# Optimization experiments

Hardware: AMD Instinct MI355X
Metric: run time of the kernel (lower is better)

The kernel has to match this reference:

```python
import jax, jax.numpy as jnp
import numpy as np

N = 8192
IN_F = 512
OUT_F = 64
ALPHA = 0.2  # LeakyReLU negative slope
NEG_INF = -9e15


def setup_inputs() -> dict:
    key = jax.random.key(0)
    k1, k2, k3, k4 = jax.random.split(key, 4)
    # xavier_uniform-style scale (gain=1.414)
    w_bound = 1.414 * np.sqrt(6.0 / (IN_F + OUT_F))
    a_bound = 1.414 * np.sqrt(6.0 / (2 * OUT_F + 1))
    return {
        "input": jax.random.normal(k1, (N, IN_F), dtype=jnp.float32),
        "adj": jax.random.randint(k2, (N, N), 0, 2, dtype=jnp.int32),
        "W": jax.random.uniform(k3, (IN_F, OUT_F), jnp.float32, -w_bound, w_bound),
        "a": jax.random.uniform(k4, (2 * OUT_F, 1), jnp.float32, -a_bound, a_bound),
        "sig_sample_size": 512,
    }


def reference(input, adj, W, a, sig_sample_size):
    h = input @ W  # [N, F]
    # Split 'a' so e_ij = leakyrelu(a1.h_i + a2.h_j) without the N*N*2F repeat/cat
    a1, a2 = a[:OUT_F, 0], a[OUT_F:, 0]  # [F], [F]
    e = jax.nn.leaky_relu((h @ a1)[:, None] + (h @ a2)[None, :], negative_slope=ALPHA)  # [N, N]
    attention = jnp.where(adj > 0, e, NEG_INF)
    attention = jax.nn.softmax(attention, axis=1)
    sig_scores = jnp.sum(attention, axis=0)  # [N]
    _, indices = jax.lax.top_k(sig_scores, sig_sample_size)
    return indices
```

## Files before the change

kernel.cpp:

```cpp
#include <hip/hip_runtime.h>
#include <stdint.h>

#define NROW 8192
#define IN_F 512
#define OUT_F 64
#define ALPHA 0.2f

typedef int int4e __attribute__((ext_vector_type(4)));

__device__ float  g_f1[NROW];
__device__ float  g_f2[NROW];
__device__ float  g_E2f[NROW];
__device__ float  g_F2f[NROW];
__device__ double g_E2d[NROW];
__device__ double g_F2d[NROW];
__device__ double g_accp[NROW];
__device__ double g_accn[NROW];
__device__ double g_colsum[NROW];
__device__ unsigned long long g_maskP[(size_t)NROW * 128];
__device__ unsigned long long g_maskN[(size_t)NROW * 128];

__global__ void __launch_bounds__(512) fused_f(const float* __restrict__ in,
                                               const float* __restrict__ W,
                                               const float* __restrict__ a) {
    __shared__ __align__(16) float wa1s[IN_F];
    __shared__ __align__(16) float wa2s[IN_F];
    int tid = threadIdx.x;
    {
        int k = tid;
        double s1 = 0.0, s2 = 0.0;
        for (int t = 0; t < OUT_F; ++t) {
            double w = (double)W[k * OUT_F + t];
            s1 += w * (double)a[t];
            s2 += w * (double)a[OUT_F + t];
        }
        wa1s[k] = (float)s1;
        wa2s[k] = (float)s2;
    }
    if (tid < 8) g_colsum[blockIdx.x * 8 + tid] = 0.0;
    __syncthreads();
    int wave = tid >> 6, lane = tid & 63;
    int row = blockIdx.x * 8 + wave;
    const float4* in4  = (const float4*)(in + (size_t)row * IN_F);
    const float4* wa14 = (const float4*)wa1s;
    const float4* wa24 = (const float4*)wa2s;
    double s1 = 0.0, s2 = 0.0;
    #pragma unroll
    for (int half = 0; half < 2; ++half) {
        int idx = half * 64 + lane;
        float4 x = in4[idx];
        float4 u = wa14[idx];
        float4 v = wa24[idx];
        s1 += (double)x.x*u.x + (double)x.y*u.y + (double)x.z*u.z + (double)x.w*u.w;
        s2 += (double)x.x*v.x + (double)x.y*v.y + (double)x.z*v.z + (double)x.w*v.w;
    }
    #pragma unroll
    for (int off = 32; off > 0; off >>= 1) {
        s1 += __shfl_down(s1, off, 64);
        s2 += __shfl_down(s2, off, 64);
    }
    if (lane == 0) {
        float f1 = (float)s1, f2 = (float)s2;
        g_f1[row] = f1; g_f2[row] = f2;
        double e2 = exp((double)f2), g2 = exp(0.2 * (double)f2);
        g_E2d[row] = e2;        g_F2d[row] = g2;
        g_E2f[row] = (float)e2; g_F2f[row] = (float)g2;
    }
}

__global__ void __launch_bounds__(256, 2) row_z_mask(const int* __restrict__ adj) {
    __shared__ float E2s[NROW];
    __shared__ float F2s[NROW];
    __shared__ double zp[16], zn[16];
    int tid = threadIdx.x;
    int wave = tid >> 6, lane = tid & 63;
    for (int k = tid; k < NROW / 4; k += 256) {
        ((float4*)E2s)[k] = ((const float4*)g_E2f)[k];
        ((float4*)F2s)[k] = ((const float4*)g_F2f)[k];
    }
    __syncthreads();
    int row0 = blockIdx.x * 4;
    for (int r = 0; r < 4; ++r) {
        int row = row0 + r;
        float f1r = g_f1[row];
        float Ft = expf(-0.2f * f1r);
        const int4e* arow = (const int4e*)(adj + (size_t)row * NROW) + wave * 512;
        int4e av[8];
        #pragma unroll
        for (int it = 0; it < 8; ++it) av[it] = arow[it * 64 + lane];
        unsigned long long mywordP = 0, mywordN = 0;
        double accp = 0.0, accn = 0.0;
        #pragma unroll
        for (int it = 0; it < 8; ++it) {
            int colbase = wave * 2048 + it * 256 + lane * 4;
            float4 E2v = *(const float4*)&E2s[colbase];
            float4 F2v = *(const float4*)&F2s[colbase];
            bool p0 = av[it].x > 0, p1 = av[it].y > 0;
            bool p2 = av[it].z > 0, p3 = av[it].w > 0;
            bool q0 = F2v.x > Ft, q1 = F2v.y > Ft, q2 = F2v.z > Ft, q3 = F2v.w > Ft;
            unsigned long long bp0 = __ballot(p0 && q0),  bn0 = __ballot(p0 && !q0);
            unsigned long long bp1 = __ballot(p1 && q1),  bn1 = __ballot(p1 && !q1);
            unsigned long long bp2 = __ballot(p2 && q2),  bn2 = __ballot(p2 && !q2);
            unsigned long long bp3 = __ballot(p3 && q3),  bn3 = __ballot(p3 && !q3);
            int bl = it * 4;
            if (lane == bl)     { mywordP = bp0; mywordN = bn0; }
            if (lane == bl + 1) { mywordP = bp1; mywordN = bn1; }
            if (lane == bl + 2) { mywordP = bp2; mywordN = bn2; }
            if (lane == bl + 3) { mywordP = bp3; mywordN = bn3; }
            accp += (p0 && q0) ? (double)E2v.x : 0.0;
            accn += (p0 && !q0) ? (double)F2v.x : 0.0;
            accp += (p1 && q1) ? (double)E2v.y : 0.0;
            accn += (p1 && !q1) ? (double)F2v.y : 0.0;
            accp += (p2 && q2) ? (double)E2v.z : 0.0;
            accn += (p2 && !q2) ? (double)F2v.z : 0.0;
            accp += (p3 && q3) ? (double)E2v.w : 0.0;
            accn += (p3 && !q3) ? (double)F2v.w : 0.0;
        }
        if (lane < 32) {
            g_maskP[(size_t)row * 128 + wave * 32 + lane] = mywordP;
            g_maskN[(size_t)row * 128 + wave * 32 + lane] = mywordN;
        }
        #pragma unroll
        for (int off = 32; off > 0; off >>= 1) {
            accp += __shfl_down(accp, off, 64);
            accn += __shfl_down(accn, off, 64);
        }
        if (lane == 0) { zp[r * 4 + wave] = accp; zn[r * 4 + wave] = accn; }
    }
    __syncthreads();
    if (tid < 4) {
        g_accp[row0 + tid] = zp[tid*4+0] + zp[tid*4+1] + zp[tid*4+2] + zp[tid*4+3];
        g_accn[row0 + tid] = zn[tid*4+0] + zn[tid*4+1] + zn[tid*4+2] + zn[tid*4+3];
    }
}

__device__ __forceinline__ unsigned long long btr64(unsigned long long x, int lane) {
    const unsigned long long hm[6] = {
        0xAAAAAAAAAAAAAAAAULL, 0xCCCCCCCCCCCCCCCCULL, 0xF0F0F0F0F0F0F0F0ULL,
        0xFF00FF00FF00FF00ULL, 0xFFFF0000FFFF0000ULL, 0xFFFFFFFF00000000ULL };
    #pragma unroll
    for (int s = 0; s < 6; ++s) {
        int d = 1 << s;
        unsigned long long y = __shfl_xor(x, d, 64);
        unsigned long long hi = hm[s];
        x = (lane & d) ? ((x & hi) | ((y >> d) & ~hi))
                       : ((x & ~hi) | ((y << d) & hi));
    }
    return x;
}

__global__ void __launch_bounds__(256) colsum_kernel() {
    __shared__ double2 GHs[256];
    int tid = threadIdx.x;
    int w = tid >> 6, lane = tid & 63;
    int cb = blockIdx.x & 31;
    int rb = blockIdx.x >> 5;
    int i0 = rb * 256;
    {
        float f1v = g_f1[i0 + tid];
        double e1 = exp((double)f1v), h1 = exp(0.2 * (double)f1v);
        double Z = e1 * g_accp[i0 + tid] + h1 * g_accn[i0 + tid];
        double zi = 1.0 / Z;
        GHs[tid] = make_double2(e1 * zi, h1 * zi);
    }
    __syncthreads();
    int glo[4], ghi[4], hlo[4], hhi[4];
    #pragma unroll
    for (int t = 0; t < 4; ++t) {
        double2 gh = GHs[t * 64 + lane];
        glo[t] = __double2loint(gh.x); ghi[t] = __double2hiint(gh.x);
        hlo[t] = __double2loint(gh.y); hhi[t] = __double2hiint(gh.y);
    }
    int W = cb * 4 + w;
    unsigned long long TP[4], TN[4];
    #pragma unroll
    for (int t = 0; t < 4; ++t) {
        unsigned long long xp = g_maskP[(size_t)(i0 + t * 64 + lane) * 128 + W];
        unsigned long long xn = g_maskN[(size_t)(i0 + t * 64 + lane) * 128 + W];
        TP[t] = btr64(xp, lane);
        TN[t] = btr64(xn, lane);
    }
    int j = (W >> 5) * 2048 + ((W >> 2) & 7) * 256 + lane * 4 + (W & 3);
    double accp = 0.0, accn = 0.0;
    #pragma unroll
    for (int t = 0; t < 4; ++t) {
        unsigned long long wp = TP[t], wn = TN[t];
        int a0 = glo[t], a1 = ghi[t], b0 = hlo[t], b1 = hhi[t];
        for (int s = 0; s < 64; ++s) {
            double G1i = __hiloint2double(__builtin_amdgcn_readlane(a1, s),
                                          __builtin_amdgcn_readlane(a0, s));
            double H1i = __hiloint2double(__builtin_amdgcn_readlane(b1, s),
                                          __builtin_amdgcn_readlane(b0, s));
            accp += ((wp >> s) & 1ULL) ? G1i : 0.0;
            accn += ((wn >> s) & 1ULL) ? H1i : 0.0;
        }
    }
    double res = g_E2d[j] * accp + g_F2d[j] * accn;
    atomicAdd(&g_colsum[j], res);
}

__global__ void __launch_bounds__(1024) topk_kernel(int* __restrict__ out, int K) {
    __shared__ unsigned int sbits[NROW];
    __shared__ unsigned int hist[256];
    __shared__ unsigned long long cand[1024];
    __shared__ unsigned long long s_prefix;
    __shared__ unsigned int s_want, s_cnt;
    int tid = threadIdx.x;
    int lane = tid & 63;
    for (int k = tid; k < NROW; k += 1024) {
        float s = (float)g_colsum[k];
        unsigned int u = __float_as_uint(s);
        u = (u & 0x80000000u) ? ~u : (u | 0x80000000u);
        sbits[k] = u;
    }
    if (tid == 0) { s_prefix = 0ULL; s_want = (unsigned)K; s_cnt = 0; }
    __syncthreads();
    for (int lvl = 0; lvl < 6; ++lvl) {
        int shift = 40 - lvl * 8;
        if (tid < 256) hist[tid] = 0;
        __syncthreads();
        unsigned long long pmask = (lvl == 0) ? 0ULL : (~0ULL << (shift + 8));
        unsigned long long prefix = s_prefix;
        for (int k = tid; k < NROW; k += 1024) {
            unsigned long long kk =
                ((unsigned long long)sbits[k] << 13) | (unsigned long long)(8191 - k);
            bool match = ((kk & pmask) == prefix);
            unsigned bb = (unsigned)(kk >> shift) & 255u;
            unsigned long long act = __ballot(match);
            unsigned long long same = act;
            #pragma unroll
            for (int t = 0; t < 8; ++t) {
                unsigned long long bt = __ballot((bb >> t) & 1u);
                same &= ((bb >> t) & 1u) ? bt : ~bt;
            }
            if (match) {
                int lead = __ffsll((long long)same) - 1;
                if (lane == lead) atomicAdd(&hist[bb], (unsigned)__popcll(same));
            }
        }
        __syncthreads();
        if (tid == 0) {
            unsigned cum = 0; int b = 255;
            for (; b >= 0; --b) { cum += hist[b]; if (cum >= s_want) break; }
            if (b < 0) b = 0;
            s_want -= (cum - hist[b]);
            s_prefix |= ((unsigned long long)b << shift);
        }
        __syncthreads();
    }
    unsigned long long thr = s_prefix;
    for (int k = tid; k < NROW; k += 1024) {
        unsigned long long kk =
            ((unsigned long long)sbits[k] << 13) | (unsigned long long)(8191 - k);
        bool keep = (kk >= thr);
        unsigned long long m = __ballot(keep);
        if (m) {
            int lead = __ffsll((long long)m) - 1;
            unsigned base = 0;
            if (lane == lead) base = atomicAdd(&s_cnt, (unsigned)__popcll(m));
            base = (unsigned)__shfl((int)base, lead, 64);
            if (keep) {
                unsigned pos = base + (unsigned)__popcll(m & ((1ULL << lane) - 1ULL));
                if (pos < 1024u) cand[pos] = kk;
            }
        }
    }
    __syncthreads();
    unsigned cnt = s_cnt;
    if ((unsigned)tid >= cnt) cand[tid] = 0ULL;
    __syncthreads();
    for (int k2 = 2; k2 <= 1024; k2 <<= 1) {
        for (int jj = k2 >> 1; jj > 0; jj >>= 1) {
            int ixj = tid ^ jj;
            if (ixj > tid) {
                unsigned long long a = cand[tid], b = cand[ixj];
                bool up = ((tid & k2) == 0);
                if (up ? (a < b) : (a > b)) { cand[tid] = b; cand[ixj] = a; }
            }
            __syncthreads();
        }
    }
    if (tid < K) out[tid] = 8191 - (int)(cand[tid] & 0x1FFFULL);
}

extern "C" void kernel_launch(void* const* d_in, const int* in_sizes, int n_in,
                              void* d_out, int out_size, void* d_ws, size_t ws_size,
                              hipStream_t stream) {
    const float* input = (const float*)d_in[0];
    const int*   adj   = (const int*)d_in[1];
    const float* W     = (const float*)d_in[2];
    const float* a     = (const float*)d_in[3];
    int* out = (int*)d_out;
    int K = out_size;

    fused_f<<<NROW / 8, 512, 0, stream>>>(input, W, a);
    row_z_mask<<<NROW / 4, 256, 0, stream>>>(adj);
    colsum_kernel<<<1024, 256, 0, stream>>>();
    topk_kernel<<<1, 1024, 0, stream>>>(out, K);
}
```

Measured before the change: 563.3 us.

## Split adjacency mask streaming from row sums and store a single mask

The row pass now streams only the adjacency and writes one bitmask instead of separate positive and negative masks. Row normalizers are computed in a new kernel that reads the mask and a permuted E/F table from shared memory. The column-sum kernel recomputes the sign of f1+f2 per element instead of loading a second mask. This halves mask write and read traffic and lightens the adjacency-streaming kernel, at the cost of two extra launches and more per-element ALU work in colsum. The sign test also changes from a comparison of exponentials to a direct sum comparison, which could classify boundary cases differently.

```diff
diff --git a/kernel.cpp b/kernel.cpp
--- a/kernel.cpp
+++ b/kernel.cpp
@@ -17,8 +17,8 @@
 __device__ double g_accp[NROW];
 __device__ double g_accn[NROW];
 __device__ double g_colsum[NROW];
-__device__ unsigned long long g_maskP[(size_t)NROW * 128];
-__device__ unsigned long long g_maskN[(size_t)NROW * 128];
+__device__ unsigned long long g_mask[(size_t)NROW * 128];
+__device__ float2 g_EFp[NROW];
 
 __global__ void __launch_bounds__(512) fused_f(const float* __restrict__ in,
                                                const float* __restrict__ W,
@@ -68,70 +68,83 @@
     }
 }
 
-__global__ void __launch_bounds__(256, 2) row_z_mask(const int* __restrict__ adj) {
-    __shared__ float E2s[NROW];
-    __shared__ float F2s[NROW];
-    __shared__ double zp[16], zn[16];
+__global__ void tbl_perm() {
+    int idx = blockIdx.x * 256 + threadIdx.x;
+    int W = idx >> 6, l = idx & 63;
+    int j = (W >> 5) * 2048 + ((W >> 2) & 7) * 256 + l * 4 + (W & 3);
+    g_EFp[idx] = make_float2(g_E2f[j], g_F2f[j]);
+}
+
+__global__ void __launch_bounds__(256) mask_stream(const int* __restrict__ adj) {
     int tid = threadIdx.x;
     int wave = tid >> 6, lane = tid & 63;
-    for (int k = tid; k < NROW / 4; k += 256) {
-        ((float4*)E2s)[k] = ((const float4*)g_E2f)[k];
-        ((float4*)F2s)[k] = ((const float4*)g_F2f)[k];
-    }
-    __syncthreads();
     int row0 = blockIdx.x * 4;
     for (int r = 0; r < 4; ++r) {
         int row = row0 + r;
-        float f1r = g_f1[row];
-        float Ft = expf(-0.2f * f1r);
         const int4e* arow = (const int4e*)(adj + (size_t)row * NROW) + wave * 512;
         int4e av[8];
         #pragma unroll
         for (int it = 0; it < 8; ++it) av[it] = arow[it * 64 + lane];
-        unsigned long long mywordP = 0, mywordN = 0;
-        double accp = 0.0, accn = 0.0;
+        unsigned long long myword = 0;
         #pragma unroll
         for (int it = 0; it < 8; ++it) {
-            int colbase = wave * 2048 + it * 256 + lane * 4;
-            float4 E2v = *(const float4*)&E2s[colbase];
-            float4 F2v = *(const float4*)&F2s[colbase];
-            bool p0 = av[it].x > 0, p1 = av[it].y > 0;
-            bool p2 = av[it].z > 0, p3 = av[it].w > 0;
-            bool q0 = F2v.x > Ft, q1 = F2v.y > Ft, q2 = F2v.z > Ft, q3 = F2v.w > Ft;
-            unsigned long long bp0 = __ballot(p0 && q0),  bn0 = __ballot(p0 && !q0);
-            unsigned long long bp1 = __ballot(p1 && q1),  bn1 = __ballot(p1 && !q1);
-            unsigned long long bp2 = __ballot(p2 && q2),  bn2 = __ballot(p2 && !q2);
-            unsigned long long bp3 = __ballot(p3 && q3),  bn3 = __ballot(p3 && !q3);
+            unsigned long long b0 = __ballot(av[it].x > 0);
+            unsigned long long b1 = __ballot(av[it].y > 0);
+            unsigned long long b2 = __ballot(av[it].z > 0);
+            unsigned long long b3 = __ballot(av[it].w > 0);
             int bl = it * 4;
-            if (lane == bl)     { mywordP = bp0; mywordN = bn0; }
-            if (lane == bl + 1) { mywordP = bp1; mywordN = bn1; }
-            if (lane == bl + 2) { mywordP = bp2; mywordN = bn2; }
-            if (lane == bl + 3) { mywordP = bp3; mywordN = bn3; }
-            accp += (p0 && q0) ? (double)E2v.x : 0.0;
-            accn += (p0 && !q0) ? (double)F2v.x : 0.0;
-            accp += (p1 && q1) ? (double)E2v.y : 0.0;
-            accn += (p1 && !q1) ? (double)F2v.y : 0.0;
-            accp += (p2 && q2) ? (double)E2v.z : 0.0;
-            accn += (p2 && !q2) ? (double)F2v.z : 0.0;
-            accp += (p3 && q3) ? (double)E2v.w : 0.0;
-            accn += (p3 && !q3) ? (double)F2v.w : 0.0;
-        }
-        if (lane < 32) {
-            g_maskP[(size_t)row * 128 + wave * 32 + lane] = mywordP;
-            g_maskN[(size_t)row * 128 + wave * 32 + lane] = mywordN;
-        }
-        #pragma unroll
-        for (int off = 32; off > 0; off >>= 1) {
-            accp += __shfl_down(accp, off, 64);
-            accn += __shfl_down(accn, off, 64);
-        }
-        if (lane == 0) { zp[r * 4 + wave] = accp; zn[r * 4 + wave] = accn; }
-    }
-    __syncthreads();
-    if (tid < 4) {
-        g_accp[row0 + tid] = zp[tid*4+0] + zp[tid*4+1] + zp[tid*4+2] + zp[tid*4+3];
-        g_accn[row0 + tid] = zn[tid*4+0] + zn[tid*4+1] + zn[tid*4+2] + zn[tid*4+3];
-    }
+            if (lane == bl)     myword = b0;
+            if (lane == bl + 1) myword = b1;
+            if (lane == bl + 2) myword = b2;
+            if (lane == bl + 3) myword = b3;
+        }
+        if (lane < 32) g_mask[(size_t)row * 128 + wave * 32 + lane] = myword;
+    }
+}
+
+__global__ void __launch_bounds__(1024) rowsum_kernel() {
+    __shared__ float2 EF[NROW];
+    int tid = threadIdx.x;
+    int wave = tid >> 6, lane = tid & 63;
+    for (int k = tid; k < NROW; k += 1024) EF[k] = g_EFp[k];
+    __syncthreads();
+    int row = blockIdx.x * 16 + wave;
+    float f1r = g_f1[row];
+    float Ft = expf(-0.2f * f1r);
+    unsigned long long wlo = g_mask[(size_t)row * 128 + lane];
+    unsigned long long whi = g_mask[(size_t)row * 128 + 64 + lane];
+    int wl0 = (int)(unsigned)wlo,        wl1 = (int)(unsigned)(wlo >> 32);
+    int wh0 = (int)(unsigned)whi,        wh1 = (int)(unsigned)(whi >> 32);
+    double accp = 0.0, accn = 0.0;
+    int half = lane >> 5, bit = lane & 31;
+    #pragma unroll
+    for (int w = 0; w < 64; ++w) {
+        unsigned lo = (unsigned)__builtin_amdgcn_readlane(wl0, w);
+        unsigned hi = (unsigned)__builtin_amdgcn_readlane(wl1, w);
+        unsigned sel = half ? hi : lo;
+        bool b = (sel >> bit) & 1u;
+        float2 ef = EF[w * 64 + lane];
+        bool q = ef.y > Ft;
+        accp += (b && q)  ? (double)ef.x : 0.0;
+        accn += (b && !q) ? (double)ef.y : 0.0;
+    }
+    #pragma unroll
+    for (int w = 0; w < 64; ++w) {
+        unsigned lo = (unsigned)__builtin_amdgcn_readlane(wh0, w);
+        unsigned hi = (unsigned)__builtin_amdgcn_readlane(wh1, w);
+        unsigned sel = half ? hi : lo;
+        bool b = (sel >> bit) & 1u;
+        float2 ef = EF[(64 + w) * 64 + lane];
+        bool q = ef.y > Ft;
+        accp += (b && q)  ? (double)ef.x : 0.0;
+        accn += (b && !q) ? (double)ef.y : 0.0;
+    }
+    #pragma unroll
+    for (int off = 32; off > 0; off >>= 1) {
+        accp += __shfl_down(accp, off, 64);
+        accn += __shfl_down(accn, off, 64);
+    }
+    if (lane == 0) { g_accp[row] = accp; g_accn[row] = accn; }
 }
 
 __device__ __forceinline__ unsigned long long btr64(unsigned long long x, int lane) {
@@ -151,48 +164,54 @@
 
 __global__ void __launch_bounds__(256) colsum_kernel() {
     __shared__ double2 GHs[256];
+    __shared__ float   f1sh[256];
     int tid = threadIdx.x;
     int w = tid >> 6, lane = tid & 63;
     int cb = blockIdx.x & 31;
     int rb = blockIdx.x >> 5;
     int i0 = rb * 256;
+    float f1v = g_f1[i0 + tid];
+    f1sh[tid] = f1v;
     {
-        float f1v = g_f1[i0 + tid];
         double e1 = exp((double)f1v), h1 = exp(0.2 * (double)f1v);
         double Z = e1 * g_accp[i0 + tid] + h1 * g_accn[i0 + tid];
         double zi = 1.0 / Z;
         GHs[tid] = make_double2(e1 * zi, h1 * zi);
     }
     __syncthreads();
-    int glo[4], ghi[4], hlo[4], hhi[4];
+    int glo[4], ghi[4], hlo[4], hhi[4], fbits[4];
     #pragma unroll
     for (int t = 0; t < 4; ++t) {
         double2 gh = GHs[t * 64 + lane];
         glo[t] = __double2loint(gh.x); ghi[t] = __double2hiint(gh.x);
         hlo[t] = __double2loint(gh.y); hhi[t] = __double2hiint(gh.y);
+        fbits[t] = __float_as_int(f1sh[t * 64 + lane]);
     }
     int W = cb * 4 + w;
-    unsigned long long TP[4], TN[4];
+    unsigned long long TP[4];
     #pragma unroll
     for (int t = 0; t < 4; ++t) {
-        unsigned long long xp = g_maskP[(size_t)(i0 + t * 64 + lane) * 128 + W];
-        unsigned long long xn = g_maskN[(size_t)(i0 + t * 64 + lane) * 128 + W];
+        unsigned long long xp = g_mask[(size_t)(i0 + t * 64 + lane) * 128 + W];
         TP[t] = btr64(xp, lane);
-        TN[t] = btr64(xn, lane);
     }
     int j = (W >> 5) * 2048 + ((W >> 2) & 7) * 256 + lane * 4 + (W & 3);
+    float f2j = g_f2[j];
     double accp = 0.0, accn = 0.0;
     #pragma unroll
     for (int t = 0; t < 4; ++t) {
-        unsigned long long wp = TP[t], wn = TN[t];
-        int a0 = glo[t], a1 = ghi[t], b0 = hlo[t], b1 = hhi[t];
+        unsigned long long wp = TP[t];
+        int a0 = glo[t], a1 = ghi[t], b0 = hlo[t], b1 = hhi[t], fb = fbits[t];
         for (int s = 0; s < 64; ++s) {
             double G1i = __hiloint2double(__builtin_amdgcn_readlane(a1, s),
                                           __builtin_amdgcn_readlane(a0, s));
             double H1i = __hiloint2double(__builtin_amdgcn_readlane(b1, s),
                                           __builtin_amdgcn_readlane(b0, s));
-            accp += ((wp >> s) & 1ULL) ? G1i : 0.0;
-            accn += ((wn >> s) & 1ULL) ? H1i : 0.0;
+            float f1i = __int_as_float(__builtin_amdgcn_readlane(fb, s));
+            bool b = (wp >> s) & 1ULL;
+            float e = f1i + f2j;
+            bool pos = e > 0.0f;
+            accp += (b && pos)  ? G1i : 0.0;
+            accn += (b && !pos) ? H1i : 0.0;
         }
     }
     double res = g_E2d[j] * accp + g_F2d[j] * accn;
@@ -294,7 +313,9 @@
     int K = out_size;
 
     fused_f<<<NROW / 8, 512, 0, stream>>>(input, W, a);
-    row_z_mask<<<NROW / 4, 256, 0, stream>>>(adj);
+    tbl_perm<<<NROW / 256, 256, 0, stream>>>();
+    mask_stream<<<NROW / 4, 256, 0, stream>>>(adj);
+    rowsum_kernel<<<NROW / 16, 1024, 0, stream>>>();
     colsum_kernel<<<1024, 256, 0, stream>>>();
     topk_kernel<<<1, 1024, 0, stream>>>(out, K);
 }
```

Measured after the change: 570.8 us. No clear change (+1.3%).
